# Optimization experiments

Measured on AMD Instinct MI355X. Metric: run time of the kernel, lower is better.

## Reference

```python
import jax, jax.numpy as jnp
import numpy as np

B, N, D_IN, D_MODEL = 8, 384, 512, 512


def gen_masking_matrix(n):
    # Vectorized port of the numba _gen_matrix: a[i, j, k] True iff k lies in the
    # 'geometric attention' reachability band between query i and key j.
    I = np.arange(n)[:, None, None]
    J = np.arange(n)[None, :, None]
    K = np.arange(n)[None, None, :]
    lt = (I < J) & (((K > I) & (K < J)) | ((K >= 2 * I - J + 1) & (K < I)))
    gt = (I > J) & (((K > J) & (K < I)) | ((K > I) & (K <= 2 * I - J)))
    return jnp.asarray(lt | gt)  # (n, n, n) bool


def setup_inputs() -> dict:
    key = jax.random.key(0)
    ks = jax.random.split(key, 8)
    s_in = 1.0 / np.sqrt(D_IN)
    return {
        "h": jax.random.normal(ks[0], (B, N, D_IN), jnp.float32),
        "mask": jnp.ones((B, N), jnp.float32),
        "Wq": jax.random.normal(ks[1], (D_MODEL, D_IN), jnp.float32) * s_in,
        "bq": jax.random.normal(ks[2], (D_MODEL,), jnp.float32) * 0.01,
        "Wk": jax.random.normal(ks[3], (D_MODEL, D_IN), jnp.float32) * s_in,
        "wlr": jax.random.normal(ks[4], (1, D_IN), jnp.float32) * s_in,
        "blr": jnp.zeros((1,), jnp.float32),
        "wrl": jax.random.normal(ks[5], (1, D_IN), jnp.float32) * s_in,
        "brl": jnp.zeros((1,), jnp.float32),
        "alpha": jnp.array([1.0 / np.sqrt(D_MODEL)], jnp.float32),
        "beta": jnp.array([1.0], jnp.float32),
        "gamma": jnp.array([0.0], jnp.float32),
        "masking_matrix": gen_masking_matrix(N),
    }


def reference(h, mask, Wq, bq, Wk, wlr, blr, wrl, brl, alpha, beta, gamma, masking_matrix):
    n = h.shape[1]
    dt = h.dtype
    q = h @ Wq.T + bq                       # (B, n, d_model)
    k = h @ Wk.T                            # (B, n, d_model)
    left = h @ wlr.T + blr                  # (B, n, 1)
    right = h @ wrl.T + brl                 # (B, n, 1)
    iu = jnp.triu(jnp.ones((n, n), dt))
    il = jnp.tril(jnp.ones((n, n), dt), -1)
    d = left * iu + right * il              # (B, n, n)
    scores = jnp.einsum("bnd,bmd->bnm", q, k)
    raw = jnp.clip(alpha * scores + beta * d + gamma, -16.0, 14.0)
    log_p = jax.nn.log_sigmoid(raw)         # log sigmoid(raw)
    log_1mp = jnp.log1p(-jnp.exp(log_p))    # log(1 - sigmoid(raw))
    # a[b,i,j] = sum_k mask[i,j,k] * log_1mp[b,i,k] + log_p[b,i,j]
    a = jnp.einsum("ijk,bik->bij", masking_matrix.astype(dt), log_1mp) + log_p
    r = a - 10000.0 * jnp.eye(n, dtype=dt)
    alignment_mask = mask[:, None, :] * mask[:, :, None]
    return r, alignment_mask
```

## Files before the change

### kernel.cpp

```cpp
#include <hip/hip_runtime.h>
#include <math.h>

#define N_SEQ 384
#define DIM 512
#define BATCH 8
#define M_ROWS (BATCH * N_SEQ)
#define QK_COLS (2 * DIM)

typedef short v8s __attribute__((ext_vector_type(8)));
typedef float v4f __attribute__((ext_vector_type(4)));

__device__ inline unsigned short f2bf(float f) {
    union { float f; unsigned u; } c; c.f = f;
    unsigned u = c.u;
    u += 0x7fffu + ((u >> 16) & 1u);
    return (unsigned short)(u >> 16);
}

#define H_F4   ((M_ROWS * DIM) / 4)
#define W_F4   ((DIM * DIM) / 4)
__global__ __launch_bounds__(256) void cast_inputs(
    const float* __restrict__ h, const float* __restrict__ Wq,
    const float* __restrict__ Wk, unsigned short* __restrict__ h_bf,
    unsigned short* __restrict__ w_bf)
{
    const int idx = blockIdx.x * 256 + threadIdx.x;
    const float4* src; unsigned short* dst; int off;
    if (idx < H_F4)            { src = (const float4*)h;  dst = h_bf;            off = idx; }
    else if (idx < H_F4 + W_F4){ src = (const float4*)Wq; dst = w_bf;            off = idx - H_F4; }
    else                       { src = (const float4*)Wk; dst = w_bf + DIM * DIM/ sizeof(short) * 2; off = idx - H_F4 - W_F4; }
    if (idx >= H_F4 + W_F4) dst = w_bf + (size_t)DIM * DIM;
    float4 v = src[off];
    ushort4 o;
    o.x = f2bf(v.x); o.y = f2bf(v.y); o.z = f2bf(v.z); o.w = f2bf(v.w);
    *(ushort4*)(dst + (size_t)off * 4) = o;
}

__global__ __launch_bounds__(256) void qk_gemm(
    const unsigned short* __restrict__ A,
    const unsigned short* __restrict__ Bm,
    const float* __restrict__ bq,
    unsigned short* __restrict__ C)
{
    __shared__ unsigned short As[128][40];
    __shared__ unsigned short Bs[128][40];
    const int bm = blockIdx.x * 128;
    const int bn = blockIdx.y * 128;
    const int t = threadIdx.x;
    const int wv = t >> 6, lane = t & 63;
    const int wm = (wv & 1) * 64, wn = (wv >> 1) * 64;
    const int lm = lane & 15, quad = lane >> 4;
    const int srow = t >> 2, skc = (t & 3) * 8;
    v4f acc[4][4] = {};
    for (int k0 = 0; k0 < DIM; k0 += 32) {
        v8s a0 = *(const v8s*)(A  + (size_t)(bm + srow)      * DIM + k0 + skc);
        v8s a1 = *(const v8s*)(A  + (size_t)(bm + srow + 64) * DIM + k0 + skc);
        v8s b0 = *(const v8s*)(Bm + (size_t)(bn + srow)      * DIM + k0 + skc);
        v8s b1 = *(const v8s*)(Bm + (size_t)(bn + srow + 64) * DIM + k0 + skc);
        __syncthreads();
        *(v8s*)&As[srow][skc]      = a0;
        *(v8s*)&As[srow + 64][skc] = a1;
        *(v8s*)&Bs[srow][skc]      = b0;
        *(v8s*)&Bs[srow + 64][skc] = b1;
        __syncthreads();
        v8s af[4], bf[4];
#pragma unroll
        for (int i = 0; i < 4; ++i) af[i] = *(const v8s*)&As[wm + i * 16 + lm][quad * 8];
#pragma unroll
        for (int j = 0; j < 4; ++j) bf[j] = *(const v8s*)&Bs[wn + j * 16 + lm][quad * 8];
#pragma unroll
        for (int i = 0; i < 4; ++i)
#pragma unroll
            for (int j = 0; j < 4; ++j)
                acc[i][j] = __builtin_amdgcn_mfma_f32_16x16x32_bf16(af[i], bf[j], acc[i][j], 0, 0, 0);
    }
#pragma unroll
    for (int i = 0; i < 4; ++i)
#pragma unroll
        for (int j = 0; j < 4; ++j) {
            const int col = bn + wn + j * 16 + lm;
            const float bias = (col < DIM) ? bq[col] : 0.f;
#pragma unroll
            for (int r = 0; r < 4; ++r) {
                const int row = bm + wm + i * 16 + quad * 4 + r;
                C[(size_t)row * QK_COLS + col] = f2bf(acc[i][j][r] + bias);
            }
        }
}

__global__ __launch_bounds__(256) void lr_gemv(
    const float* __restrict__ h, const float* __restrict__ wlr,
    const float* __restrict__ blr, const float* __restrict__ wrl,
    const float* __restrict__ brl, float* __restrict__ left,
    float* __restrict__ right)
{
    const int row  = blockIdx.x * 4 + (threadIdx.x >> 6);
    const int lane = threadIdx.x & 63;
    const float* hr = h + (size_t)row * DIM;
    float sl = 0.f, sr = 0.f;
    for (int c = lane; c < DIM; c += 64) {
        const float hv = hr[c];
        sl = fmaf(hv, wlr[c], sl);
        sr = fmaf(hv, wrl[c], sr);
    }
#pragma unroll
    for (int off = 32; off > 0; off >>= 1) {
        sl += __shfl_down(sl, off);
        sr += __shfl_down(sr, off);
    }
    if (lane == 0) {
        left[row]  = sl + blr[0];
        right[row] = sr + brl[0];
    }
}

__global__ __launch_bounds__(256) void score_gemm(
    const unsigned short* __restrict__ QK, const float* __restrict__ left,
    const float* __restrict__ right, const float* __restrict__ alpha,
    const float* __restrict__ beta, const float* __restrict__ gamma,
    float* __restrict__ raw)
{
    __shared__ unsigned short As[64][40];
    __shared__ unsigned short Bs[64][40];
    const int b  = blockIdx.z;
    const int bi = blockIdx.x * 64, bj = blockIdx.y * 64;
    const int t = threadIdx.x;
    const int wv = t >> 6, lane = t & 63;
    const int wm = (wv & 1) * 32, wn = (wv >> 1) * 32;
    const int lm = lane & 15, quad = lane >> 4;
    const int srow = t >> 2, skc = (t & 3) * 8;
    const unsigned short* qb = QK + (size_t)(b * N_SEQ) * QK_COLS;
    v4f acc[2][2] = {};
    for (int k0 = 0; k0 < DIM; k0 += 32) {
        v8s a0 = *(const v8s*)(qb + (size_t)(bi + srow) * QK_COLS + k0 + skc);
        v8s b0 = *(const v8s*)(qb + (size_t)(bj + srow) * QK_COLS + DIM + k0 + skc);
        __syncthreads();
        *(v8s*)&As[srow][skc] = a0;
        *(v8s*)&Bs[srow][skc] = b0;
        __syncthreads();
        v8s af[2], bf[2];
#pragma unroll
        for (int i = 0; i < 2; ++i) af[i] = *(const v8s*)&As[wm + i * 16 + lm][quad * 8];
#pragma unroll
        for (int j = 0; j < 2; ++j) bf[j] = *(const v8s*)&Bs[wn + j * 16 + lm][quad * 8];
#pragma unroll
        for (int i = 0; i < 2; ++i)
#pragma unroll
            for (int j = 0; j < 2; ++j)
                acc[i][j] = __builtin_amdgcn_mfma_f32_16x16x32_bf16(af[i], bf[j], acc[i][j], 0, 0, 0);
    }
    const float al = alpha[0], be = beta[0], ga = gamma[0];
#pragma unroll
    for (int i = 0; i < 2; ++i)
#pragma unroll
        for (int j = 0; j < 2; ++j) {
            const int jcol = bj + wn + j * 16 + lm;
#pragma unroll
            for (int r = 0; r < 4; ++r) {
                const int irow = bi + wm + i * 16 + quad * 4 + r;
                const float lv = left[b * N_SEQ + irow];
                const float rv = right[b * N_SEQ + irow];
                const float dterm = (jcol >= irow) ? lv : rv;
                float v = fmaf(al, acc[i][j][r], fmaf(be, dterm, ga));
                v = fminf(fmaxf(v, -16.f), 14.f);
                raw[((size_t)b * N_SEQ + irow) * N_SEQ + jcol] = v;
            }
        }
}

__global__ __launch_bounds__(384) void finalize(
    const float* __restrict__ raw, const float* __restrict__ mask,
    float* __restrict__ out_r, float* __restrict__ out_am)
{
    const int n = N_SEQ;
    const int i = blockIdx.x;
    const int b = blockIdx.y;
    const int j = threadIdx.x;
    __shared__ float P[N_SEQ + 1];
    __shared__ float wsum[6];
    const float x  = raw[((size_t)b * n + i) * n + j];
    const float lp = -log1pf(expf(-x));
    const float l1 = -log1pf(expf(x));
    const int lane = j & 63, w = j >> 6;
    float v = l1;
#pragma unroll
    for (int off = 1; off < 64; off <<= 1) {
        const float tt = __shfl_up(v, off);
        if (lane >= off) v += tt;
    }
    if (lane == 63) wsum[w] = v;
    __syncthreads();
    float woff = 0.f;
    for (int t = 0; t < w; ++t) woff += wsum[t];
    P[j + 1] = v + woff;
    if (j == 0) P[0] = 0.f;
    __syncthreads();
    float s = 0.f;
    if (i < j) {
        int lo2 = 2 * i - j + 1; if (lo2 < 0) lo2 = 0;
        s = (P[j] - P[i + 1]) + (P[i] - P[lo2]);
    } else if (i > j) {
        int hi2 = 2 * i - j + 1; if (hi2 > n) hi2 = n;
        s = (P[i] - P[j + 1]) + (P[hi2] - P[i + 1]);
    }
    float r = s + lp;
    if (i == j) r -= 10000.f;
    const size_t o = ((size_t)b * n + i) * n + j;
    out_r[o]  = r;
    out_am[o] = mask[b * n + i] * mask[b * n + j];
}

extern "C" void kernel_launch(void* const* d_in, const int* in_sizes, int n_in,
                              void* d_out, int out_size, void* d_ws, size_t ws_size,
                              hipStream_t stream) {
    const float* h     = (const float*)d_in[0];
    const float* mask  = (const float*)d_in[1];
    const float* Wq    = (const float*)d_in[2];
    const float* bq    = (const float*)d_in[3];
    const float* Wk    = (const float*)d_in[4];
    const float* wlr   = (const float*)d_in[5];
    const float* blr   = (const float*)d_in[6];
    const float* wrl   = (const float*)d_in[7];
    const float* brl   = (const float*)d_in[8];
    const float* alpha = (const float*)d_in[9];
    const float* beta  = (const float*)d_in[10];
    const float* gamma = (const float*)d_in[11];

    unsigned short* h_bf  = (unsigned short*)d_ws;
    unsigned short* w_bf  = h_bf + (size_t)M_ROWS * DIM;
    unsigned short* qk_bf = w_bf + (size_t)QK_COLS * DIM;
    float* left  = (float*)(qk_bf + (size_t)M_ROWS * QK_COLS);
    float* right = left + M_ROWS;
    float* raw   = right + M_ROWS;

    float* out_r  = (float*)d_out;
    float* out_am = out_r + (size_t)BATCH * N_SEQ * N_SEQ;

    cast_inputs<<<(H_F4 + 2 * W_F4) / 256, 256, 0, stream>>>(h, Wq, Wk, h_bf, w_bf);
    lr_gemv<<<M_ROWS / 4, 256, 0, stream>>>(h, wlr, blr, wrl, brl, left, right);
    dim3 g1(M_ROWS / 128, QK_COLS / 128);
    qk_gemm<<<g1, 256, 0, stream>>>(h_bf, w_bf, bq, qk_bf);
    dim3 g2(N_SEQ / 64, N_SEQ / 64, BATCH);
    score_gemm<<<g2, 256, 0, stream>>>(qk_bf, left, right, alpha, beta, gamma, raw);
    dim3 g3(N_SEQ, BATCH);
    finalize<<<g3, 384, 0, stream>>>(raw, mask, out_r, out_am);
}
```

Before: 316.8 us.

## Fuse left/right GEMV, score GEMM and prefix-sum finalize into one kernel

Merges three kernels into a single score_finalize kernel. Each block handles 16 query rows of one batch against all 384 keys. It computes the left/right projections for its rows, runs the QK^T MFMA with the full key tile staged in shared memory, writes the clipped raw scores to LDS, and does the log-sigmoid prefix-sum finalize in place. This drops the global round trip of the raw score matrix and the left/right buffers, plus two kernel launches. In exchange the grid shrinks to 192 blocks, each block reloads all K rows with low MFMA reuse (one A fragment per wave), and LDS use is about 32KB per block, which may limit occupancy.

```diff
diff --git a/kernel.cpp b/kernel.cpp
--- a/kernel.cpp
+++ b/kernel.cpp
@@ -6,6 +6,7 @@
 #define BATCH 8
 #define M_ROWS (BATCH * N_SEQ)
 #define QK_COLS (2 * DIM)
+#define TI 16
 
 typedef short v8s __attribute__((ext_vector_type(8)));
 typedef float v4f __attribute__((ext_vector_type(4)));
@@ -17,23 +18,22 @@
     return (unsigned short)(u >> 16);
 }
 
-#define H_F4   ((M_ROWS * DIM) / 4)
-#define W_F4   ((DIM * DIM) / 4)
+#define H_F4 ((M_ROWS * DIM) / 4)
+#define W_F4 ((DIM * DIM) / 4)
 __global__ __launch_bounds__(256) void cast_inputs(
     const float* __restrict__ h, const float* __restrict__ Wq,
     const float* __restrict__ Wk, unsigned short* __restrict__ h_bf,
     unsigned short* __restrict__ w_bf)
 {
     const int idx = blockIdx.x * 256 + threadIdx.x;
-    const float4* src; unsigned short* dst; int off;
-    if (idx < H_F4)            { src = (const float4*)h;  dst = h_bf;            off = idx; }
-    else if (idx < H_F4 + W_F4){ src = (const float4*)Wq; dst = w_bf;            off = idx - H_F4; }
-    else                       { src = (const float4*)Wk; dst = w_bf + DIM * DIM/ sizeof(short) * 2; off = idx - H_F4 - W_F4; }
-    if (idx >= H_F4 + W_F4) dst = w_bf + (size_t)DIM * DIM;
+    const float4* src; unsigned short* dst; size_t off;
+    if (idx < H_F4)             { src = (const float4*)h;  dst = h_bf;                     off = idx; }
+    else if (idx < H_F4 + W_F4) { src = (const float4*)Wq; dst = w_bf;                     off = idx - H_F4; }
+    else                        { src = (const float4*)Wk; dst = w_bf + (size_t)DIM * DIM; off = idx - H_F4 - W_F4; }
     float4 v = src[off];
     ushort4 o;
     o.x = f2bf(v.x); o.y = f2bf(v.y); o.z = f2bf(v.z); o.w = f2bf(v.w);
-    *(ushort4*)(dst + (size_t)off * 4) = o;
+    *(ushort4*)(dst + off * 4) = o;
 }
 
 __global__ __launch_bounds__(256) void qk_gemm(
@@ -88,126 +88,130 @@
         }
 }
 
-__global__ __launch_bounds__(256) void lr_gemv(
-    const float* __restrict__ h, const float* __restrict__ wlr,
-    const float* __restrict__ blr, const float* __restrict__ wrl,
-    const float* __restrict__ brl, float* __restrict__ left,
-    float* __restrict__ right)
-{
-    const int row  = blockIdx.x * 4 + (threadIdx.x >> 6);
-    const int lane = threadIdx.x & 63;
-    const float* hr = h + (size_t)row * DIM;
-    float sl = 0.f, sr = 0.f;
-    for (int c = lane; c < DIM; c += 64) {
-        const float hv = hr[c];
-        sl = fmaf(hv, wlr[c], sl);
-        sr = fmaf(hv, wrl[c], sr);
-    }
-#pragma unroll
-    for (int off = 32; off > 0; off >>= 1) {
-        sl += __shfl_down(sl, off);
-        sr += __shfl_down(sr, off);
-    }
-    if (lane == 0) {
-        left[row]  = sl + blr[0];
-        right[row] = sr + brl[0];
-    }
-}
-
-__global__ __launch_bounds__(256) void score_gemm(
-    const unsigned short* __restrict__ QK, const float* __restrict__ left,
-    const float* __restrict__ right, const float* __restrict__ alpha,
-    const float* __restrict__ beta, const float* __restrict__ gamma,
-    float* __restrict__ raw)
-{
-    __shared__ unsigned short As[64][40];
-    __shared__ unsigned short Bs[64][40];
-    const int b  = blockIdx.z;
-    const int bi = blockIdx.x * 64, bj = blockIdx.y * 64;
-    const int t = threadIdx.x;
-    const int wv = t >> 6, lane = t & 63;
-    const int wm = (wv & 1) * 32, wn = (wv >> 1) * 32;
-    const int lm = lane & 15, quad = lane >> 4;
-    const int srow = t >> 2, skc = (t & 3) * 8;
-    const unsigned short* qb = QK + (size_t)(b * N_SEQ) * QK_COLS;
-    v4f acc[2][2] = {};
-    for (int k0 = 0; k0 < DIM; k0 += 32) {
-        v8s a0 = *(const v8s*)(qb + (size_t)(bi + srow) * QK_COLS + k0 + skc);
-        v8s b0 = *(const v8s*)(qb + (size_t)(bj + srow) * QK_COLS + DIM + k0 + skc);
-        __syncthreads();
-        *(v8s*)&As[srow][skc] = a0;
-        *(v8s*)&Bs[srow][skc] = b0;
-        __syncthreads();
-        v8s af[2], bf[2];
-#pragma unroll
-        for (int i = 0; i < 2; ++i) af[i] = *(const v8s*)&As[wm + i * 16 + lm][quad * 8];
-#pragma unroll
-        for (int j = 0; j < 2; ++j) bf[j] = *(const v8s*)&Bs[wn + j * 16 + lm][quad * 8];
-#pragma unroll
-        for (int i = 0; i < 2; ++i)
-#pragma unroll
-            for (int j = 0; j < 2; ++j)
-                acc[i][j] = __builtin_amdgcn_mfma_f32_16x16x32_bf16(af[i], bf[j], acc[i][j], 0, 0, 0);
-    }
-    const float al = alpha[0], be = beta[0], ga = gamma[0];
-#pragma unroll
-    for (int i = 0; i < 2; ++i)
-#pragma unroll
-        for (int j = 0; j < 2; ++j) {
-            const int jcol = bj + wn + j * 16 + lm;
-#pragma unroll
-            for (int r = 0; r < 4; ++r) {
-                const int irow = bi + wm + i * 16 + quad * 4 + r;
-                const float lv = left[b * N_SEQ + irow];
-                const float rv = right[b * N_SEQ + irow];
-                const float dterm = (jcol >= irow) ? lv : rv;
-                float v = fmaf(al, acc[i][j][r], fmaf(be, dterm, ga));
-                v = fminf(fmaxf(v, -16.f), 14.f);
-                raw[((size_t)b * N_SEQ + irow) * N_SEQ + jcol] = v;
-            }
-        }
-}
-
-__global__ __launch_bounds__(384) void finalize(
-    const float* __restrict__ raw, const float* __restrict__ mask,
+__global__ __launch_bounds__(256) void score_finalize(
+    const unsigned short* __restrict__ QK, const float* __restrict__ h,
+    const float* __restrict__ wlr, const float* __restrict__ blr,
+    const float* __restrict__ wrl, const float* __restrict__ brl,
+    const float* __restrict__ alpha, const float* __restrict__ beta,
+    const float* __restrict__ gamma, const float* __restrict__ mask,
     float* __restrict__ out_r, float* __restrict__ out_am)
 {
-    const int n = N_SEQ;
-    const int i = blockIdx.x;
-    const int b = blockIdx.y;
-    const int j = threadIdx.x;
-    __shared__ float P[N_SEQ + 1];
-    __shared__ float wsum[6];
-    const float x  = raw[((size_t)b * n + i) * n + j];
-    const float lp = -log1pf(expf(-x));
-    const float l1 = -log1pf(expf(x));
-    const int lane = j & 63, w = j >> 6;
-    float v = l1;
-#pragma unroll
-    for (int off = 1; off < 64; off <<= 1) {
-        const float tt = __shfl_up(v, off);
-        if (lane >= off) v += tt;
-    }
-    if (lane == 63) wsum[w] = v;
+    __shared__ __align__(16) char smem[32000];
+    __shared__ float lrL[TI], lrR[TI];
+    unsigned short (*As)[40]  = (unsigned short(*)[40])smem;
+    unsigned short (*Bs)[40]  = (unsigned short(*)[40])(smem + 1280);
+    float (*rawS)[385]        = (float(*)[385])smem;
+    float (*P)[385]           = (float(*)[385])(smem + 24640);
+
+    const int b  = blockIdx.y;
+    const int i0 = blockIdx.x * TI;
+    const int t  = threadIdx.x;
+    const int wv = t >> 6, lane = t & 63;
+    const int lm = lane & 15, quad = lane >> 4;
+
+#pragma unroll
+    for (int rr = 0; rr < 4; ++rr) {
+        const int r = wv * 4 + rr;
+        const float* hr = h + (size_t)(b * N_SEQ + i0 + r) * DIM;
+        float sl = 0.f, sr = 0.f;
+        for (int c = lane; c < DIM; c += 64) {
+            const float hv = hr[c];
+            sl = fmaf(hv, wlr[c], sl);
+            sr = fmaf(hv, wrl[c], sr);
+        }
+#pragma unroll
+        for (int off = 32; off > 0; off >>= 1) {
+            sl += __shfl_down(sl, off);
+            sr += __shfl_down(sr, off);
+        }
+        if (lane == 0) { lrL[r] = sl + blr[0]; lrR[r] = sr + brl[0]; }
+    }
+
+    v4f acc[6] = {};
+    const unsigned short* qbase = QK + (size_t)(b * N_SEQ + i0) * QK_COLS;
+    const unsigned short* kbase = QK + (size_t)(b * N_SEQ) * QK_COLS + DIM;
+    const int srow = t >> 2, skc = (t & 3) * 8;
+    for (int k0 = 0; k0 < DIM; k0 += 32) {
+        v8s breg[6];
+#pragma unroll
+        for (int s = 0; s < 6; ++s)
+            breg[s] = *(const v8s*)(kbase + (size_t)(s * 64 + srow) * QK_COLS + k0 + skc);
+        v8s areg = {};
+        if (t < 64) areg = *(const v8s*)(qbase + (size_t)(t >> 2) * QK_COLS + k0 + skc);
+        __syncthreads();
+#pragma unroll
+        for (int s = 0; s < 6; ++s) *(v8s*)&Bs[s * 64 + srow][skc] = breg[s];
+        if (t < 64) *(v8s*)&As[t >> 2][skc] = areg;
+        __syncthreads();
+        const v8s af = *(const v8s*)&As[lm][quad * 8];
+#pragma unroll
+        for (int j = 0; j < 6; ++j) {
+            const v8s bf = *(const v8s*)&Bs[(wv * 6 + j) * 16 + lm][quad * 8];
+            acc[j] = __builtin_amdgcn_mfma_f32_16x16x32_bf16(af, bf, acc[j], 0, 0, 0);
+        }
+    }
     __syncthreads();
-    float woff = 0.f;
-    for (int t = 0; t < w; ++t) woff += wsum[t];
-    P[j + 1] = v + woff;
-    if (j == 0) P[0] = 0.f;
+
+    const float al = alpha[0], be = beta[0], ga = gamma[0];
+#pragma unroll
+    for (int j = 0; j < 6; ++j) {
+        const int col = (wv * 6 + j) * 16 + lm;
+#pragma unroll
+        for (int r4 = 0; r4 < 4; ++r4) {
+            const int rloc = quad * 4 + r4;
+            const int ig = i0 + rloc;
+            const float dterm = (col >= ig) ? lrL[rloc] : lrR[rloc];
+            float v = fmaf(al, acc[j][r4], fmaf(be, dterm, ga));
+            v = fminf(fmaxf(v, -16.f), 14.f);
+            rawS[rloc][col] = v;
+        }
+    }
     __syncthreads();
-    float s = 0.f;
-    if (i < j) {
-        int lo2 = 2 * i - j + 1; if (lo2 < 0) lo2 = 0;
-        s = (P[j] - P[i + 1]) + (P[i] - P[lo2]);
-    } else if (i > j) {
-        int hi2 = 2 * i - j + 1; if (hi2 > n) hi2 = n;
-        s = (P[i] - P[j + 1]) + (P[hi2] - P[i + 1]);
-    }
-    float r = s + lp;
-    if (i == j) r -= 10000.f;
-    const size_t o = ((size_t)b * n + i) * n + j;
-    out_r[o]  = r;
-    out_am[o] = mask[b * n + i] * mask[b * n + j];
+
+#pragma unroll
+    for (int rr = 0; rr < 4; ++rr) {
+        const int rloc = wv * 4 + rr;
+        const int ig = i0 + rloc;
+        float x[6], l1[6], s6[6];
+        float T = 0.f;
+#pragma unroll
+        for (int c = 0; c < 6; ++c) {
+            x[c] = rawS[rloc][lane * 6 + c];
+            l1[c] = -log1pf(expf(x[c]));
+            T += l1[c];
+            s6[c] = T;
+        }
+        float incl = T;
+#pragma unroll
+        for (int off = 1; off < 64; off <<= 1) {
+            const float tt = __shfl_up(incl, off);
+            if (lane >= off) incl += tt;
+        }
+        const float E = incl - T;
+#pragma unroll
+        for (int c = 0; c < 6; ++c) P[wv][1 + lane * 6 + c] = E + s6[c];
+        if (lane == 0) P[wv][0] = 0.f;
+        __syncthreads();
+        const float maskbi = mask[b * N_SEQ + ig];
+#pragma unroll
+        for (int c = 0; c < 6; ++c) {
+            const int j = lane * 6 + c;
+            float S = 0.f;
+            if (ig < j) {
+                int lo2 = 2 * ig - j + 1; if (lo2 < 0) lo2 = 0;
+                S = (P[wv][j] - P[wv][ig + 1]) + (P[wv][ig] - P[wv][lo2]);
+            } else if (ig > j) {
+                int hi2 = 2 * ig - j + 1; if (hi2 > N_SEQ) hi2 = N_SEQ;
+                S = (P[wv][ig] - P[wv][j + 1]) + (P[wv][hi2] - P[wv][ig + 1]);
+            }
+            float rv = S + (x[c] + l1[c]);
+            if (ig == j) rv -= 10000.f;
+            const size_t o = (size_t)(b * N_SEQ + ig) * N_SEQ + j;
+            out_r[o]  = rv;
+            out_am[o] = maskbi * mask[b * N_SEQ + j];
+        }
+        __syncthreads();
+    }
 }
 
 extern "C" void kernel_launch(void* const* d_in, const int* in_sizes, int n_in,
@@ -229,19 +233,14 @@
     unsigned short* h_bf  = (unsigned short*)d_ws;
     unsigned short* w_bf  = h_bf + (size_t)M_ROWS * DIM;
     unsigned short* qk_bf = w_bf + (size_t)QK_COLS * DIM;
-    float* left  = (float*)(qk_bf + (size_t)M_ROWS * QK_COLS);
-    float* right = left + M_ROWS;
-    float* raw   = right + M_ROWS;
 
     float* out_r  = (float*)d_out;
     float* out_am = out_r + (size_t)BATCH * N_SEQ * N_SEQ;
 
     cast_inputs<<<(H_F4 + 2 * W_F4) / 256, 256, 0, stream>>>(h, Wq, Wk, h_bf, w_bf);
-    lr_gemv<<<M_ROWS / 4, 256, 0, stream>>>(h, wlr, blr, wrl, brl, left, right);
     dim3 g1(M_ROWS / 128, QK_COLS / 128);
     qk_gemm<<<g1, 256, 0, stream>>>(h_bf, w_bf, bq, qk_bf);
-    dim3 g2(N_SEQ / 64, N_SEQ / 64, BATCH);
-    score_gemm<<<g2, 256, 0, stream>>>(qk_bf, left, right, alpha, beta, gamma, raw);
-    dim3 g3(N_SEQ, BATCH);
-    finalize<<<g3, 384, 0, stream>>>(raw, mask, out_r, out_am);
-}
+    dim3 g2(N_SEQ / TI, BATCH);
+    score_finalize<<<g2, 256, 0, stream>>>(qk_bf, h, wlr, blr, wrl, brl,
+                                           alpha, beta, gamma, mask, out_r, out_am);
+}
```

Result: slower. 330.5 us (+4.3%).
